# Optimization experiments

Measured on AMD Instinct MI355X. Metric: run time of the kernel, lower is better.

## Reference

```python
import jax, jax.numpy as jnp
from jax import lax
import numpy as np

NZ = 1000        # latent / probability-vector size
TRUNC = 50       # self.truncation
C = 50.0         # self.c
EPS = 1e-5       # BatchNorm eps (PyTorch default)


def _conv_transpose(x, w, b, stride, pad):
    """PyTorch ConvTranspose2d. w: (in_ch, out_ch, kh, kw), x: NCHW."""
    k = w.shape[2]
    # flip spatially, swap in/out -> OIHW kernel for a dilated forward conv
    w_eff = jnp.transpose(jnp.flip(w, (2, 3)), (1, 0, 2, 3))
    p = k - 1 - pad
    y = lax.conv_general_dilated(
        x, w_eff, window_strides=(1, 1), padding=[(p, p), (p, p)],
        lhs_dilation=(stride, stride),
        dimension_numbers=("NCHW", "OIHW", "NCHW"))
    return y + b[None, :, None, None]


def _batchnorm(x, gamma, beta):
    # training-mode BN: batch statistics over (N, H, W), biased variance
    m = x.mean((0, 2, 3), keepdims=True)
    v = ((x - m) ** 2).mean((0, 2, 3), keepdims=True)
    xn = (x - m) * lax.rsqrt(v + EPS)
    return xn * gamma[None, :, None, None] + beta[None, :, None, None]


def setup_inputs() -> dict:
    key = jax.random.key(0)
    ks = jax.random.split(key, 8)
    B = 2048
    s = 0.02
    inp = {
        "x": jax.random.uniform(ks[0], (B, NZ), jnp.float32),
        "w1": jax.random.normal(ks[1], (NZ, 512, 4, 4), jnp.float32) * s,
        "b1": jnp.zeros((512,), jnp.float32),
        "g1": jnp.ones((512,), jnp.float32),
        "be1": jnp.zeros((512,), jnp.float32),
        "w2": jax.random.normal(ks[2], (512, 256, 4, 4), jnp.float32) * s,
        "b2": jnp.zeros((256,), jnp.float32),
        "g2": jnp.ones((256,), jnp.float32),
        "be2": jnp.zeros((256,), jnp.float32),
        "w3": jax.random.normal(ks[3], (256, 128, 4, 4), jnp.float32) * s,
        "b3": jnp.zeros((128,), jnp.float32),
        "g3": jnp.ones((128,), jnp.float32),
        "be3": jnp.zeros((128,), jnp.float32),
        "w4": jax.random.normal(ks[4], (128, 1, 4, 4), jnp.float32) * s,
        "b4": jnp.zeros((1,), jnp.float32),
    }
    return inp


def reference(x, w1, b1, g1, be1, w2, b2, g2, be2, w3, b3, g3, be3, w4, b4):
    B = x.shape[0]
    # truncation_vector: topk -> clamp(log)+c -> shift nonneg -> scatter
    top_k, idx = lax.top_k(x, TRUNC)                      # [B, TRUNC]
    top_k = jnp.maximum(jnp.log(top_k), -1000.0) + C
    top_k = top_k + jax.nn.relu(-top_k.min(1, keepdims=True))
    z = jnp.zeros((B, NZ), x.dtype).at[jnp.arange(B)[:, None], idx].set(top_k)

    h = z.reshape(B, NZ, 1, 1)
    h = jnp.tanh(_batchnorm(_conv_transpose(h, w1, b1, 1, 0), g1, be1))  # [B,512,4,4]
    h = jnp.tanh(_batchnorm(_conv_transpose(h, w2, b2, 2, 1), g2, be2))  # [B,256,8,8]
    h = jnp.tanh(_batchnorm(_conv_transpose(h, w3, b3, 2, 1), g3, be3))  # [B,128,16,16]
    h = jax.nn.sigmoid(_conv_transpose(h, w4, b4, 2, 1))                 # [B,1,32,32]
    return h.reshape(B, 1, 32, 32)
```

## Files before the change

### kernel.cpp

```cpp
#include <hip/hip_runtime.h>
#include <cstdint>
#include <cstddef>


typedef unsigned short u16;
typedef unsigned int u32;
typedef __attribute__((ext_vector_type(8))) short s16x8;
typedef __attribute__((ext_vector_type(16))) float f32x16;

static __device__ __forceinline__ float bf2f(u16 u) {
  union { u32 i; float f; } v; v.i = ((u32)u) << 16; return v.f;
}
static __device__ __forceinline__ u16 f2bf(float f) {
  union { float f; u32 i; } v; v.f = f;
  const u32 r = v.i + 0x7fffu + ((v.i >> 16) & 1u);
  return (u16)(r >> 16);
}
static __device__ __forceinline__ void lds_barrier() {
  asm volatile("s_waitcnt lgkmcnt(0)" ::: "memory");
  __builtin_amdgcn_s_barrier();
}

__global__ __launch_bounds__(256) void topk_kernel(const float* __restrict__ x,
                                                   float* __restrict__ vals,
                                                   int* __restrict__ idxs) {
  const int lane = threadIdx.x & 63;
  const int b = blockIdx.x * 4 + (threadIdx.x >> 6);
  float v[16];
  #pragma unroll
  for (int j = 0; j < 16; ++j) {
    const int idx = lane + 64 * j;
    v[j] = (idx < 1000) ? x[(size_t)b * 1000 + idx] : -INFINITY;
  }
  float keepv = 1.0f;
  int keepi = 0;
  for (int k = 0; k < 50; ++k) {
    float bv = v[0]; int bj = 0;
    #pragma unroll
    for (int j = 1; j < 16; ++j)
      if (v[j] > bv) { bv = v[j]; bj = j; }
    int bi = lane + 64 * bj;
    #pragma unroll
    for (int off = 1; off < 64; off <<= 1) {
      const float ov = __shfl_xor(bv, off);
      const int oi = __shfl_xor(bi, off);
      if (ov > bv || (ov == bv && oi < bi)) { bv = ov; bi = oi; }
    }
    const int slot = bi >> 6;
    const bool own = (lane == (bi & 63));
    #pragma unroll
    for (int j = 0; j < 16; ++j)
      if (own && slot == j) v[j] = -INFINITY;
    if (lane == k) { keepv = bv; keepi = bi; }
  }
  const float tk = fmaxf(logf(keepv), -1000.0f) + 50.0f;
  float m = (lane < 50) ? tk : INFINITY;
  #pragma unroll
  for (int off = 1; off < 64; off <<= 1) m = fminf(m, __shfl_xor(m, off));
  const float shift = fmaxf(-m, 0.0f);
  if (lane < 50) {
    vals[b * 50 + lane] = tk + shift;
    idxs[b * 50 + lane] = keepi;
  }
}

__global__ __launch_bounds__(256) void w1t_kernel(const float* __restrict__ w1,
                                                  u16* __restrict__ w1t) {
  const int cin = blockIdx.x;
  const int t = threadIdx.x;
  __shared__ float is[512 * 17];
  const float* src = w1 + (size_t)cin * 8192;
  #pragma unroll
  for (int r = 0; r < 8; ++r) {
    const int f = r * 1024 + t * 4;
    const float4 v = *reinterpret_cast<const float4*>(src + f);
    const int co = f >> 4, s = f & 15;
    is[co * 17 + s + 0] = v.x;
    is[co * 17 + s + 1] = v.y;
    is[co * 17 + s + 2] = v.z;
    is[co * 17 + s + 3] = v.w;
  }
  __syncthreads();
  u16* dst = w1t + (size_t)cin * 8192;
  #pragma unroll
  for (int p = 0; p < 4; ++p) {
    const int i8 = (p * 256 + t) * 8;
    const int s = i8 >> 9, co = i8 & 511;
    union { u16 h[8]; s16x8 v; } pk;
    #pragma unroll
    for (int q = 0; q < 8; ++q) pk.h[q] = f2bf(is[(co + q) * 17 + s]);
    *reinterpret_cast<s16x8*>(dst + i8) = pk.v;
  }
}

template <int CIN, int COUT>
__global__ __launch_bounds__(256) void wt2_kernel(const float* __restrict__ w,
                                                  u16* __restrict__ wt2,
                                                  int obase, int NCH) {
  constexpr int KB = CIN / 16;
  const int kb = blockIdx.x;
  const int chg = blockIdx.y;
  const int t = threadIdx.x;
  __shared__ __align__(16) u16 tile[16 * 32 * 16];
  for (int i = t; i < 512; i += 256) {
    const int kk = i >> 5;
    const int ch = i & 31;
    const float* src = w + ((size_t)(kb * 16 + kk) * COUT + obase + chg * 32 + ch) * 16;
    #pragma unroll
    for (int q4 = 0; q4 < 4; ++q4) {
      const float4 v = *reinterpret_cast<const float4*>(src + q4 * 4);
      tile[(q4 * 4 + 0) * 512 + ch * 16 + kk] = f2bf(v.x);
      tile[(q4 * 4 + 1) * 512 + ch * 16 + kk] = f2bf(v.y);
      tile[(q4 * 4 + 2) * 512 + ch * 16 + kk] = f2bf(v.z);
      tile[(q4 * 4 + 3) * 512 + ch * 16 + kk] = f2bf(v.w);
    }
  }
  __syncthreads();
  for (int i = t; i < 16 * 64; i += 256) {
    const int tap = i >> 6;
    const int off = (i & 63) * 8;
    u16* dst = wt2 + ((size_t)(tap * KB + kb) * NCH + chg * 32) * 16 + off;
    *reinterpret_cast<s16x8*>(dst) = *reinterpret_cast<const s16x8*>(tile + tap * 512 + off);
  }
}

__global__ __launch_bounds__(256) void conv1_kernel(const float* __restrict__ vals,
                                                    const int* __restrict__ idxs,
                                                    const u16* __restrict__ w1t,
                                                    const float* __restrict__ b1,
                                                    u16* __restrict__ y1) {
  const int b = blockIdx.x;
  const int t = threadIdx.x;
  __shared__ float sval[50];
  __shared__ int sidx[50];
  if (t < 50) { sval[t] = vals[b * 50 + t]; sidx[t] = idxs[b * 50 + t]; }
  __syncthreads();
  const int co = (t & 63) * 8;
  const int s0 = t >> 6;
  float b8[8];
  #pragma unroll
  for (int q = 0; q < 8; ++q) b8[q] = b1[co + q];
  #pragma unroll
  for (int sp = 0; sp < 4; ++sp) {
    const int s = sp * 4 + s0;
    float acc[8] = {0.f, 0.f, 0.f, 0.f, 0.f, 0.f, 0.f, 0.f};
    for (int j = 0; j < 50; ++j) {
      const float v = sval[j];
      union { s16x8 v8; u16 h[8]; } w;
      w.v8 = *reinterpret_cast<const s16x8*>(w1t + (size_t)sidx[j] * 8192 + s * 512 + co);
      #pragma unroll
      for (int q = 0; q < 8; ++q) acc[q] = fmaf(v, bf2f(w.h[q]), acc[q]);
    }
    union { u16 h[8]; s16x8 v8; } o;
    #pragma unroll
    for (int q = 0; q < 8; ++q) o.h[q] = f2bf(acc[q] + b8[q]);
    *reinterpret_cast<s16x8*>(y1 + (size_t)b * 8192 + s * 512 + co) = o.v8;
  }
}

__global__ __launch_bounds__(256) void bnstats_kernel(const u16* __restrict__ y,
                                                      float* __restrict__ sp,
                                                      float* __restrict__ sqp,
                                                      int C, int CB, int ROWS) {
  const int PB = CB >> 1;
  const int PR = 256 / PB;
  const int t = threadIdx.x;
  const int cp = t & (PB - 1);
  const int rl = t / PB;
  const int cbase = blockIdx.x * CB;
  const int split = blockIdx.y;
  const int RPB = ROWS >> 7;
  const u16* base = y + (size_t)split * RPB * C + cbase + 2 * cp;
  float s0 = 0.f, s1 = 0.f, q0 = 0.f, q1 = 0.f;
  for (int r = rl; r < RPB; r += PR) {
    const u32 raw = *reinterpret_cast<const u32*>(base + (size_t)r * C);
    const float a = bf2f((u16)(raw & 0xffffu));
    const float b = bf2f((u16)(raw >> 16));
    s0 += a; s1 += b;
    q0 = fmaf(a, a, q0); q1 = fmaf(b, b, q1);
  }
  __shared__ float4 arr[256];
  arr[t] = make_float4(s0, s1, q0, q1);
  __syncthreads();
  if (t < PB) {
    float4 acc = arr[t];
    for (int g = 1; g < PR; ++g) {
      const float4 v = arr[g * PB + t];
      acc.x += v.x; acc.y += v.y; acc.z += v.z; acc.w += v.w;
    }
    const int c = cbase + 2 * t;
    sp[split * C + c] = acc.x;
    sp[split * C + c + 1] = acc.y;
    sqp[split * C + c] = acc.z;
    sqp[split * C + c + 1] = acc.w;
  }
}

__global__ __launch_bounds__(256) void bnfin_kernel(const float* __restrict__ sp,
                                                    const float* __restrict__ sqp,
                                                    const float* __restrict__ g,
                                                    const float* __restrict__ be,
                                                    float* __restrict__ a,
                                                    float* __restrict__ bb,
                                                    int logC, int SPLITS, float inv) {
  const int t = threadIdx.x;
  const int C = 1 << logC;
  const int lc = t & (C - 1);
  int PARTS = 256 >> logC;
  if (PARTS == 0) PARTS = 1;
  const int part = (logC >= 8) ? 0 : (t >> logC);
  const int chunk = SPLITS / PARTS;
  const int c = (blockIdx.x << 8) + lc;
  float s = 0.f, s2 = 0.f;
  for (int k = part * chunk; k < (part + 1) * chunk; ++k) {
    s += sp[(size_t)k * C + c];
    s2 += sqp[(size_t)k * C + c];
  }
  __shared__ float rs[256], rq[256];
  rs[t] = s; rq[t] = s2;
  __syncthreads();
  if (part == 0 && t < C) {
    for (int p = 1; p < PARTS; ++p) {
      s += rs[(p << logC) + lc];
      s2 += rq[(p << logC) + lc];
    }
    const float m = s * inv;
    float var = fmaf(-m, m, s2 * inv);
    var = fmaxf(var, 0.f);
    const float r = 1.0f / sqrtf(var + 1e-5f);
    const float av = g[c] * r;
    a[c] = av;
    bb[c] = fmaf(-m, av, be[c]);
  }
}

__global__ __launch_bounds__(256) void bnact_kernel(u16* __restrict__ y,
                                                    const float* __restrict__ a,
                                                    const float* __restrict__ bb,
                                                    int Cm1) {
  const size_t i = ((size_t)blockIdx.x * 256 + threadIdx.x) * 8;
  const int c = (int)i & Cm1;
  uint4 raw = *reinterpret_cast<uint4*>(y + i);
  float av[8], bv[8];
  *reinterpret_cast<float4*>(av) = *reinterpret_cast<const float4*>(a + c);
  *reinterpret_cast<float4*>(av + 4) = *reinterpret_cast<const float4*>(a + c + 4);
  *reinterpret_cast<float4*>(bv) = *reinterpret_cast<const float4*>(bb + c);
  *reinterpret_cast<float4*>(bv + 4) = *reinterpret_cast<const float4*>(bb + c + 4);
  u32 w[4] = {raw.x, raw.y, raw.z, raw.w};
  #pragma unroll
  for (int q = 0; q < 4; ++q) {
    const float lo = tanhf(fmaf(bf2f((u16)(w[q] & 0xffffu)), av[2 * q], bv[2 * q]));
    const float hi = tanhf(fmaf(bf2f((u16)(w[q] >> 16)), av[2 * q + 1], bv[2 * q + 1]));
    w[q] = (u32)f2bf(lo) | ((u32)f2bf(hi) << 16);
  }
  raw.x = w[0]; raw.y = w[1]; raw.z = w[2]; raw.w = w[3];
  *reinterpret_cast<uint4*>(y + i) = raw;
}

template <int SIN, int CIN, int WM, int WN, int MBATCH, int COUT_STORE>
__global__ __launch_bounds__(512, 2) void convt_mfma(const u16* __restrict__ in,
                                                     const u16* __restrict__ wt,
                                                     const float* __restrict__ bias,
                                                     u16* __restrict__ outp,
                                                     float* __restrict__ spp,
                                                     float* __restrict__ sqpp,
                                                     int o_gbase) {
  constexpr int SS = SIN * SIN;
  constexpr int MB = MBATCH * SS;
  constexpr int NB = WN * 32;
  constexpr int KB = CIN / 16;
  constexpr int LOGS = (SIN == 4) ? 2 : 3;
  constexpr int NPASS = MB / 64;
  constexpr int NSTEP = CIN / 64;
  constexpr int BUFW = (MB + 1) * 64;
  constexpr int KYT[2][2] = {{1, 3}, {2, 0}};
  constexpr int DYT[2][2] = {{0, -1}, {0, 1}};
  static_assert(WM * WN == 8, "8 waves");
  static_assert(MB == WM * 32, "MFR==1");
  __shared__ __align__(16) u16 As[2 * BUFW];
  __shared__ float sred[512];

  const int t = threadIdx.x;
  const int lane = t & 63;
  const int wave = t >> 6;
  const int wn = wave % WN;
  const int wm = wave / WN;
  const int l31 = lane & 31;
  const int kl2 = lane >> 5;
  const int bx = blockIdx.x;
  const int R0 = blockIdx.y * MB;
  const int NCHT = gridDim.x * NB;

  int rb[9];
  {
    const int r = wm * 32 + l31;
    const int bl = r >> (2 * LOGS);
    const int rr = r & (SS - 1);
    const int sy = rr >> LOGS, sx = rr & (SIN - 1);
    #pragma unroll
    for (int dyi = 0; dyi < 3; ++dyi)
      #pragma unroll
      for (int dxi = 0; dxi < 3; ++dxi) {
        const int ny = sy + dyi - 1, nx = sx + dxi - 1;
        const bool ok = (ny >= 0 && ny < SIN && nx >= 0 && nx < SIN);
        const int rp = ok ? ((bl << (2 * LOGS)) + (ny << LOGS) + nx) : MB;
        rb[dyi * 3 + dxi] = (rp << 7) | ((rp & 7) << 4);
      }
  }
  if (t < 16) {
    s16x8 z = {};
    const int buf = t >> 3;
    *reinterpret_cast<s16x8*>(As + buf * BUFW + MB * 64 + (t & 7) * 8) = z;
  }

  f32x16 acc[2][2];
  #pragma unroll
  for (int py = 0; py < 2; ++py)
    #pragma unroll
    for (int px = 0; px < 2; ++px) acc[py][px] = (f32x16)(0.f);

  const int chb = bx * NB + wn * 32;
  const int ocw = chb + l31;
  const u16* wlane = wt + (size_t)(chb + l31) * 16 + kl2 * 8;
  const size_t nstride = (size_t)NCHT * 16;

  const int srow = t >> 3;
  const int scol = (t & 7) * 8;
  const u16* gsrc = in + (size_t)(R0 + srow) * CIN + scol;

  s16x8 sreg[NPASS];
  #pragma unroll
  for (int p = 0; p < NPASS; ++p)
    sreg[p] = *reinterpret_cast<const s16x8*>(gsrc + (size_t)p * 64 * CIN);

  int cur = 0;
  for (int s = 0; s < NSTEP; ++s) {
    u16* dbuf = As + cur * BUFW;
    #pragma unroll
    for (int p = 0; p < NPASS; ++p) {
      const int row = p * 64 + srow;
      const int db = row * 128 + ((scol * 2) ^ ((row & 7) << 4));
      *reinterpret_cast<s16x8*>((char*)dbuf + db) = sreg[p];
    }
    if (s + 1 < NSTEP) {
      const u16* gn = gsrc + (s + 1) * 64;
      #pragma unroll
      for (int p = 0; p < NPASS; ++p)
        sreg[p] = *reinterpret_cast<const s16x8*>(gn + (size_t)p * 64 * CIN);
    }
    lds_barrier();

    const u16* Ab = As + cur * BUFW;
    #pragma unroll
    for (int ksub = 0; ksub < 4; ++ksub) {
      const int kb = s * 4 + ksub;
      s16x8 bf[2][2][2][2];
      #pragma unroll
      for (int py = 0; py < 2; ++py)
        #pragma unroll
        for (int px = 0; px < 2; ++px)
          #pragma unroll
          for (int jy = 0; jy < 2; ++jy)
            #pragma unroll
            for (int jx = 0; jx < 2; ++jx) {
              const int tap = KYT[py][jy] * 4 + KYT[px][jx];
              bf[py][px][jy][jx] = *reinterpret_cast<const s16x8*>(
                  wlane + (size_t)(tap * KB + kb) * nstride);
            }
      const int koff = ksub * 32 + kl2 * 16;
      s16x8 af[9];
      #pragma unroll
      for (int s9 = 0; s9 < 9; ++s9)
        af[s9] = *reinterpret_cast<const s16x8*>((const char*)Ab + (rb[s9] ^ koff));
      __builtin_amdgcn_s_setprio(1);
      #pragma unroll
      for (int py = 0; py < 2; ++py)
        #pragma unroll
        for (int px = 0; px < 2; ++px)
          #pragma unroll
          for (int jy = 0; jy < 2; ++jy)
            #pragma unroll
            for (int jx = 0; jx < 2; ++jx) {
              const int s9 = (DYT[py][jy] + 1) * 3 + (DYT[px][jx] + 1);
              acc[py][px] = __builtin_amdgcn_mfma_f32_32x32x16_bf16(
                  af[s9], bf[py][px][jy][jx], acc[py][px], 0, 0, 0);
            }
      __builtin_amdgcn_s_setprio(0);
    }
    cur ^= 1;
  }

  const float bo = bias[o_gbase + ocw];
  const int B0 = blockIdx.y * MBATCH;
  float s_ = 0.f, q_ = 0.f;
  #pragma unroll
  for (int i = 0; i < 16; ++i) {
    const int rl_ = (i & 3) + 8 * (i >> 2) + 4 * kl2;
    const int r = wm * 32 + rl_;
    const int bl = r >> (2 * LOGS);
    const int rr = r & (SS - 1);
    const int sy = rr >> LOGS, sx = rr & (SIN - 1);
    const size_t ob = (size_t)(B0 + bl) * 4 * SS;
    #pragma unroll
    for (int py = 0; py < 2; ++py)
      #pragma unroll
      for (int px = 0; px < 2; ++px) {
        const int od = (2 * sy + py) * (2 * SIN) + 2 * sx + px;
        const float v = acc[py][px][i] + bo;
        s_ += v;
        q_ = fmaf(v, v, q_);
        outp[(ob + od) * COUT_STORE + ocw] = f2bf(v);
      }
  }
  s_ += __shfl_xor(s_, 32);
  q_ += __shfl_xor(q_, 32);
  if (lane < 32) {
    sred[wave * 32 + l31] = s_;
    sred[256 + wave * 32 + l31] = q_;
  }
  __syncthreads();
  if (t < WN * 32) {
    const int wnr = t >> 5;
    const int ch = t & 31;
    float ss = 0.f, qq = 0.f;
    #pragma unroll
    for (int w = 0; w < WM; ++w) {
      ss += sred[(w * WN + wnr) * 32 + ch];
      qq += sred[256 + (w * WN + wnr) * 32 + ch];
    }
    const int c = bx * NB + wnr * 32 + ch;
    spp[(size_t)blockIdx.y * COUT_STORE + c] = ss;
    sqpp[(size_t)blockIdx.y * COUT_STORE + c] = qq;
  }
}

__global__ __launch_bounds__(256) void conv4_kernel(const u16* __restrict__ h3c,
                                                    const float* __restrict__ ac,
                                                    const float* __restrict__ bc,
                                                    const float* __restrict__ w4,
                                                    const float* __restrict__ b4,
                                                    float* __restrict__ outp,
                                                    int cbase, int last) {
  const int b = blockIdx.x;
  const int t = threadIdx.x;
  __shared__ float wsh[32 * 16];
  __shared__ float is[32 * 257];
  for (int i = t; i < 512; i += 256) wsh[i] = w4[cbase * 16 + i];
  const int cq = (t & 3) * 8;
  float av[8], bv[8];
  *reinterpret_cast<float4*>(av)     = *reinterpret_cast<const float4*>(ac + cq);
  *reinterpret_cast<float4*>(av + 4) = *reinterpret_cast<const float4*>(ac + cq + 4);
  *reinterpret_cast<float4*>(bv)     = *reinterpret_cast<const float4*>(bc + cq);
  *reinterpret_cast<float4*>(bv + 4) = *reinterpret_cast<const float4*>(bc + cq + 4);
  #pragma unroll
  for (int p = 0; p < 4; ++p) {
    const int idx8 = p * 256 + t;
    const int s = idx8 >> 2;
    union { s16x8 v8; u16 h[8]; } r;
    r.v8 = *reinterpret_cast<const s16x8*>(h3c + ((size_t)b * 256 + s) * 32 + cq);
    #pragma unroll
    for (int q = 0; q < 8; ++q)
      is[(cq + q) * 257 + s] = tanhf(fmaf(bf2f(r.h[q]), av[q], bv[q]));
  }
  __syncthreads();
  float acc[4] = {0.f, 0.f, 0.f, 0.f};
  const int ox = t & 31;
  const int oy0 = t >> 5;
  for (int c = 0; c < 32; ++c) {
    #pragma unroll
    for (int k = 0; k < 4; ++k) {
      const int oy = oy0 + 8 * k;
      #pragma unroll
      for (int jy = 0; jy < 2; ++jy) {
        const int ky = 2 * jy + 1 - (oy & 1);
        const int iyn = oy + 1 - ky;
        if ((unsigned)iyn < 32u) {
          const int iy = iyn >> 1;
          #pragma unroll
          for (int jx = 0; jx < 2; ++jx) {
            const int kx = 2 * jx + 1 - (ox & 1);
            const int ixn = ox + 1 - kx;
            if ((unsigned)ixn < 32u) {
              const int ix = ixn >> 1;
              acc[k] = fmaf(is[c * 257 + iy * 16 + ix], wsh[c * 16 + ky * 4 + kx], acc[k]);
            }
          }
        }
      }
    }
  }
  #pragma unroll
  for (int k = 0; k < 4; ++k) {
    const int oy = oy0 + 8 * k;
    const size_t ob = (size_t)b * 1024 + oy * 32 + ox;
    const float base = (cbase == 0) ? b4[0] : outp[ob];
    const float v = base + acc[k];
    outp[ob] = last ? (1.0f / (1.0f + expf(-v))) : v;
  }
}

extern "C" void kernel_launch(void* const* d_in, const int* in_sizes, int n_in,
                              void* d_out, int out_size, void* d_ws, size_t ws_size,
                              hipStream_t stream) {
  (void)in_sizes; (void)n_in; (void)out_size; (void)ws_size;
  const float* x   = (const float*)d_in[0];
  const float* w1  = (const float*)d_in[1];
  const float* b1  = (const float*)d_in[2];
  const float* g1  = (const float*)d_in[3];
  const float* be1 = (const float*)d_in[4];
  const float* w2  = (const float*)d_in[5];
  const float* b2  = (const float*)d_in[6];
  const float* g2  = (const float*)d_in[7];
  const float* be2 = (const float*)d_in[8];
  const float* w3  = (const float*)d_in[9];
  const float* b3  = (const float*)d_in[10];
  const float* g3  = (const float*)d_in[11];
  const float* be3 = (const float*)d_in[12];
  const float* w4  = (const float*)d_in[13];
  const float* b4  = (const float*)d_in[14];

  char* ws = (char*)d_ws;
  u16*   y2   = (u16*)(ws + 0);
  u16*   y1   = (u16*)(ws + 67108864);
  u16*   y3c  = (u16*)(ws + 100663296);
  u16*   w1t  = (u16*)(ws + 100663296);
  u16*   w2t  = (u16*)(ws + 117047296);
  float* vals = (float*)(ws + 134217728);
  int*   idxs = (int*)(ws + 134627328);
  float* sp   = (float*)(ws + 134217728);
  float* sqp  = (float*)(ws + 134479872);
  float* ac   = (float*)(ws + 134742016);
  float* bc   = (float*)(ws + 134744064);
  u16*   w3tc = (u16*)(ws + 134746112);
  float* outp = (float*)d_out;

  w1t_kernel<<<1000, 256, 0, stream>>>(w1, w1t);
  wt2_kernel<512, 256><<<dim3(32, 8), 256, 0, stream>>>(w2, w2t, 0, 256);
  topk_kernel<<<512, 256, 0, stream>>>(x, vals, idxs);

  conv1_kernel<<<2048, 256, 0, stream>>>(vals, idxs, w1t, b1, y1);
  bnstats_kernel<<<dim3(4, 128), 256, 0, stream>>>(y1, sp, sqp, 512, 128, 32768);
  bnfin_kernel<<<2, 256, 0, stream>>>(sp, sqp, g1, be1, ac, bc, 9, 128, 1.0f / 32768.0f);
  bnact_kernel<<<8192, 256, 0, stream>>>(y1, ac, bc, 511);

  convt_mfma<4, 512, 4, 2, 8, 256><<<dim3(4, 256), 512, 0, stream>>>(
      y1, w2t, b2, y2, sp, sqp, 0);
  bnfin_kernel<<<1, 256, 0, stream>>>(sp, sqp, g2, be2, ac, bc, 8, 256, 1.0f / 131072.0f);
  bnact_kernel<<<16384, 256, 0, stream>>>(y2, ac, bc, 255);

  for (int ch = 0; ch < 4; ++ch) {
    const int cb = ch * 32;
    wt2_kernel<256, 128><<<dim3(16, 1), 256, 0, stream>>>(w3, w3tc, cb, 32);
    convt_mfma<8, 256, 8, 1, 4, 32><<<dim3(1, 512), 512, 0, stream>>>(
        y2, w3tc, b3, y3c, sp, sqp, cb);
    bnfin_kernel<<<1, 256, 0, stream>>>(sp, sqp, g3 + cb, be3 + cb, ac, bc, 5, 512,
                                        1.0f / 524288.0f);
    conv4_kernel<<<2048, 256, 0, stream>>>(y3c, ac, bc, w4, b4, outp, cb, ch == 3);
  }
}
```

Baseline: 1.120 ms.

## Shrink MFMA conv tiles to 4 waves, software-pipeline B loads, chunk layer3 by 64

The transposed-conv MFMA kernel now uses 256-thread blocks (4 waves) with smaller M tiles, giving more blocks. Weight fragments are loaded per output phase with double-buffered prefetch instead of all 16 up front, which lowers register pressure. Layer 3 is processed in two 64-channel chunks instead of four 32-channel chunks, with BN statistics moved to a separate bnstats pass and conv4 templated on channel count. Smaller tiles give less reuse of weights per block, and the extra stats kernel adds another read of y3c.

After: 1.510 ms. +34.8%, slower.

```diff
diff --git a/kernel.cpp b/kernel.cpp
--- a/kernel.cpp
+++ b/kernel.cpp
@@ -161,7 +161,7 @@
 __global__ __launch_bounds__(256) void bnstats_kernel(const u16* __restrict__ y,
                                                       float* __restrict__ sp,
                                                       float* __restrict__ sqp,
-                                                      int C, int CB, int ROWS) {
+                                                      int C, int CB, long long ROWS) {
   const int PB = CB >> 1;
   const int PR = 256 / PB;
   const int t = threadIdx.x;
@@ -169,10 +169,10 @@
   const int rl = t / PB;
   const int cbase = blockIdx.x * CB;
   const int split = blockIdx.y;
-  const int RPB = ROWS >> 7;
+  const long long RPB = ROWS >> 7;
   const u16* base = y + (size_t)split * RPB * C + cbase + 2 * cp;
   float s0 = 0.f, s1 = 0.f, q0 = 0.f, q1 = 0.f;
-  for (int r = rl; r < RPB; r += PR) {
+  for (long long r = rl; r < RPB; r += PR) {
     const u32 raw = *reinterpret_cast<const u32*>(base + (size_t)r * C);
     const float a = bf2f((u16)(raw & 0xffffu));
     const float b = bf2f((u16)(raw >> 16));
@@ -257,28 +257,28 @@
   *reinterpret_cast<uint4*>(y + i) = raw;
 }
 
-template <int SIN, int CIN, int WM, int WN, int MBATCH, int COUT_STORE>
-__global__ __launch_bounds__(512, 2) void convt_mfma(const u16* __restrict__ in,
-                                                     const u16* __restrict__ wt,
-                                                     const float* __restrict__ bias,
-                                                     u16* __restrict__ outp,
-                                                     float* __restrict__ spp,
-                                                     float* __restrict__ sqpp,
-                                                     int o_gbase) {
+template <int SIN, int CIN, int WM, int WN, int MBATCH, int COUT_STORE, bool STATS>
+__global__ __launch_bounds__(256) void convt_mfma(const u16* __restrict__ in,
+                                                  const u16* __restrict__ wt,
+                                                  const float* __restrict__ bias,
+                                                  u16* __restrict__ outp,
+                                                  float* __restrict__ spp,
+                                                  float* __restrict__ sqpp,
+                                                  int o_gbase) {
   constexpr int SS = SIN * SIN;
   constexpr int MB = MBATCH * SS;
   constexpr int NB = WN * 32;
   constexpr int KB = CIN / 16;
   constexpr int LOGS = (SIN == 4) ? 2 : 3;
-  constexpr int NPASS = MB / 64;
+  constexpr int NPASS = MB / 32;
   constexpr int NSTEP = CIN / 64;
   constexpr int BUFW = (MB + 1) * 64;
   constexpr int KYT[2][2] = {{1, 3}, {2, 0}};
   constexpr int DYT[2][2] = {{0, -1}, {0, 1}};
-  static_assert(WM * WN == 8, "8 waves");
+  static_assert(WM * WN == 4, "4 waves");
   static_assert(MB == WM * 32, "MFR==1");
   __shared__ __align__(16) u16 As[2 * BUFW];
-  __shared__ float sred[512];
+  __shared__ float sred[256];
 
   const int t = threadIdx.x;
   const int lane = t & 63;
@@ -331,14 +331,14 @@
   s16x8 sreg[NPASS];
   #pragma unroll
   for (int p = 0; p < NPASS; ++p)
-    sreg[p] = *reinterpret_cast<const s16x8*>(gsrc + (size_t)p * 64 * CIN);
+    sreg[p] = *reinterpret_cast<const s16x8*>(gsrc + (size_t)p * 32 * CIN);
 
   int cur = 0;
   for (int s = 0; s < NSTEP; ++s) {
     u16* dbuf = As + cur * BUFW;
     #pragma unroll
     for (int p = 0; p < NPASS; ++p) {
-      const int row = p * 64 + srow;
+      const int row = p * 32 + srow;
       const int db = row * 128 + ((scol * 2) ^ ((row & 7) << 4));
       *reinterpret_cast<s16x8*>((char*)dbuf + db) = sreg[p];
     }
@@ -346,7 +346,7 @@
       const u16* gn = gsrc + (s + 1) * 64;
       #pragma unroll
       for (int p = 0; p < NPASS; ++p)
-        sreg[p] = *reinterpret_cast<const s16x8*>(gn + (size_t)p * 64 * CIN);
+        sreg[p] = *reinterpret_cast<const s16x8*>(gn + (size_t)p * 32 * CIN);
     }
     lds_barrier();
 
@@ -354,38 +354,43 @@
     #pragma unroll
     for (int ksub = 0; ksub < 4; ++ksub) {
       const int kb = s * 4 + ksub;
-      s16x8 bf[2][2][2][2];
-      #pragma unroll
-      for (int py = 0; py < 2; ++py)
-        #pragma unroll
-        for (int px = 0; px < 2; ++px)
-          #pragma unroll
-          for (int jy = 0; jy < 2; ++jy)
-            #pragma unroll
-            for (int jx = 0; jx < 2; ++jx) {
-              const int tap = KYT[py][jy] * 4 + KYT[px][jx];
-              bf[py][px][jy][jx] = *reinterpret_cast<const s16x8*>(
-                  wlane + (size_t)(tap * KB + kb) * nstride);
-            }
+      const u16* wkb = wlane + (size_t)kb * nstride;
       const int koff = ksub * 32 + kl2 * 16;
       s16x8 af[9];
       #pragma unroll
       for (int s9 = 0; s9 < 9; ++s9)
         af[s9] = *reinterpret_cast<const s16x8*>((const char*)Ab + (rb[s9] ^ koff));
-      __builtin_amdgcn_s_setprio(1);
-      #pragma unroll
-      for (int py = 0; py < 2; ++py)
+      s16x8 bq0[4], bq1[4];
+      #pragma unroll
+      for (int j = 0; j < 4; ++j) {
+        const int tap = KYT[0][j >> 1] * 4 + KYT[0][j & 1];
+        bq0[j] = *reinterpret_cast<const s16x8*>(wkb + (size_t)tap * KB * nstride);
+      }
+      #pragma unroll
+      for (int q = 0; q < 4; ++q) {
+        const int py = q >> 1, px = q & 1;
+        if (q < 3) {
+          const int nq = q + 1;
+          const int npy = nq >> 1, npx = nq & 1;
+          s16x8* nb = (nq & 1) ? bq1 : bq0;
+          #pragma unroll
+          for (int j = 0; j < 4; ++j) {
+            const int tap = KYT[npy][j >> 1] * 4 + KYT[npx][j & 1];
+            nb[j] = *reinterpret_cast<const s16x8*>(wkb + (size_t)tap * KB * nstride);
+          }
+        }
+        const s16x8* cb = (q & 1) ? bq1 : bq0;
+        __builtin_amdgcn_s_setprio(1);
         #pragma unroll
-        for (int px = 0; px < 2; ++px)
+        for (int jy = 0; jy < 2; ++jy)
           #pragma unroll
-          for (int jy = 0; jy < 2; ++jy)
-            #pragma unroll
-            for (int jx = 0; jx < 2; ++jx) {
-              const int s9 = (DYT[py][jy] + 1) * 3 + (DYT[px][jx] + 1);
-              acc[py][px] = __builtin_amdgcn_mfma_f32_32x32x16_bf16(
-                  af[s9], bf[py][px][jy][jx], acc[py][px], 0, 0, 0);
-            }
-      __builtin_amdgcn_s_setprio(0);
+          for (int jx = 0; jx < 2; ++jx) {
+            const int s9 = (DYT[py][jy] + 1) * 3 + (DYT[px][jx] + 1);
+            acc[py][px] = __builtin_amdgcn_mfma_f32_32x32x16_bf16(
+                af[s9], cb[jy * 2 + jx], acc[py][px], 0, 0, 0);
+          }
+        __builtin_amdgcn_s_setprio(0);
+      }
     }
     cur ^= 1;
   }
@@ -412,28 +417,31 @@
         outp[(ob + od) * COUT_STORE + ocw] = f2bf(v);
       }
   }
-  s_ += __shfl_xor(s_, 32);
-  q_ += __shfl_xor(q_, 32);
-  if (lane < 32) {
-    sred[wave * 32 + l31] = s_;
-    sred[256 + wave * 32 + l31] = q_;
-  }
-  __syncthreads();
-  if (t < WN * 32) {
-    const int wnr = t >> 5;
-    const int ch = t & 31;
-    float ss = 0.f, qq = 0.f;
-    #pragma unroll
-    for (int w = 0; w < WM; ++w) {
-      ss += sred[(w * WN + wnr) * 32 + ch];
-      qq += sred[256 + (w * WN + wnr) * 32 + ch];
-    }
-    const int c = bx * NB + wnr * 32 + ch;
-    spp[(size_t)blockIdx.y * COUT_STORE + c] = ss;
-    sqpp[(size_t)blockIdx.y * COUT_STORE + c] = qq;
-  }
-}
-
+  if constexpr (STATS) {
+    s_ += __shfl_xor(s_, 32);
+    q_ += __shfl_xor(q_, 32);
+    if (lane < 32) {
+      sred[wave * 32 + l31] = s_;
+      sred[128 + wave * 32 + l31] = q_;
+    }
+    __syncthreads();
+    if (t < WN * 32) {
+      const int wnr = t >> 5;
+      const int ch = t & 31;
+      float ss = 0.f, qq = 0.f;
+      #pragma unroll
+      for (int w = 0; w < WM; ++w) {
+        ss += sred[(w * WN + wnr) * 32 + ch];
+        qq += sred[128 + (w * WN + wnr) * 32 + ch];
+      }
+      const int c = bx * NB + wnr * 32 + ch;
+      spp[(size_t)blockIdx.y * COUT_STORE + c] = ss;
+      sqpp[(size_t)blockIdx.y * COUT_STORE + c] = qq;
+    }
+  }
+}
+
+template <int NCH>
 __global__ __launch_bounds__(256) void conv4_kernel(const u16* __restrict__ h3c,
                                                     const float* __restrict__ ac,
                                                     const float* __restrict__ bc,
@@ -443,21 +451,22 @@
                                                     int cbase, int last) {
   const int b = blockIdx.x;
   const int t = threadIdx.x;
-  __shared__ float wsh[32 * 16];
-  __shared__ float is[32 * 257];
-  for (int i = t; i < 512; i += 256) wsh[i] = w4[cbase * 16 + i];
-  const int cq = (t & 3) * 8;
+  __shared__ float wsh[NCH * 16];
+  __shared__ float is[NCH * 257];
+  for (int i = t; i < NCH * 16; i += 256) wsh[i] = w4[cbase * 16 + i];
+  constexpr int CG = NCH / 8;
+  const int cq = (t & (CG - 1)) * 8;
   float av[8], bv[8];
   *reinterpret_cast<float4*>(av)     = *reinterpret_cast<const float4*>(ac + cq);
   *reinterpret_cast<float4*>(av + 4) = *reinterpret_cast<const float4*>(ac + cq + 4);
   *reinterpret_cast<float4*>(bv)     = *reinterpret_cast<const float4*>(bc + cq);
   *reinterpret_cast<float4*>(bv + 4) = *reinterpret_cast<const float4*>(bc + cq + 4);
   #pragma unroll
-  for (int p = 0; p < 4; ++p) {
-    const int idx8 = p * 256 + t;
-    const int s = idx8 >> 2;
+  for (int p = 0; p < CG; ++p) {
+    const int i8 = p * 256 + t;
+    const int s = i8 / CG;
     union { s16x8 v8; u16 h[8]; } r;
-    r.v8 = *reinterpret_cast<const s16x8*>(h3c + ((size_t)b * 256 + s) * 32 + cq);
+    r.v8 = *reinterpret_cast<const s16x8*>(h3c + ((size_t)b * 256 + s) * NCH + cq);
     #pragma unroll
     for (int q = 0; q < 8; ++q)
       is[(cq + q) * 257 + s] = tanhf(fmaf(bf2f(r.h[q]), av[q], bv[q]));
@@ -466,7 +475,7 @@
   float acc[4] = {0.f, 0.f, 0.f, 0.f};
   const int ox = t & 31;
   const int oy0 = t >> 5;
-  for (int c = 0; c < 32; ++c) {
+  for (int c = 0; c < NCH; ++c) {
     #pragma unroll
     for (int k = 0; k < 4; ++k) {
       const int oy = oy0 + 8 * k;
@@ -522,16 +531,20 @@
   char* ws = (char*)d_ws;
   u16*   y2   = (u16*)(ws + 0);
   u16*   y1   = (u16*)(ws + 67108864);
-  u16*   y3c  = (u16*)(ws + 100663296);
+  u16*   y3c  = (u16*)(ws + 67108864);
   u16*   w1t  = (u16*)(ws + 100663296);
+  float* sp2  = (float*)(ws + 100663296);
+  float* sqp2 = (float*)(ws + 101187584);
   u16*   w2t  = (u16*)(ws + 117047296);
   float* vals = (float*)(ws + 134217728);
   int*   idxs = (int*)(ws + 134627328);
-  float* sp   = (float*)(ws + 134217728);
-  float* sqp  = (float*)(ws + 134479872);
+  float* sp1  = (float*)(ws + 134217728);
+  float* sqp1 = (float*)(ws + 134479872);
+  u16*   w3tc = (u16*)(ws + 134217728);
   float* ac   = (float*)(ws + 134742016);
   float* bc   = (float*)(ws + 134744064);
-  u16*   w3tc = (u16*)(ws + 134746112);
+  float* sp3  = (float*)(ws + 134746112);
+  float* sqp3 = (float*)(ws + 134778880);
   float* outp = (float*)d_out;
 
   w1t_kernel<<<1000, 256, 0, stream>>>(w1, w1t);
@@ -539,22 +552,23 @@
   topk_kernel<<<512, 256, 0, stream>>>(x, vals, idxs);
 
   conv1_kernel<<<2048, 256, 0, stream>>>(vals, idxs, w1t, b1, y1);
-  bnstats_kernel<<<dim3(4, 128), 256, 0, stream>>>(y1, sp, sqp, 512, 128, 32768);
-  bnfin_kernel<<<2, 256, 0, stream>>>(sp, sqp, g1, be1, ac, bc, 9, 128, 1.0f / 32768.0f);
+  bnstats_kernel<<<dim3(4, 128), 256, 0, stream>>>(y1, sp1, sqp1, 512, 128, 32768);
+  bnfin_kernel<<<2, 256, 0, stream>>>(sp1, sqp1, g1, be1, ac, bc, 9, 128, 1.0f / 32768.0f);
   bnact_kernel<<<8192, 256, 0, stream>>>(y1, ac, bc, 511);
 
-  convt_mfma<4, 512, 4, 2, 8, 256><<<dim3(4, 256), 512, 0, stream>>>(
-      y1, w2t, b2, y2, sp, sqp, 0);
-  bnfin_kernel<<<1, 256, 0, stream>>>(sp, sqp, g2, be2, ac, bc, 8, 256, 1.0f / 131072.0f);
+  convt_mfma<4, 512, 2, 2, 4, 256, true><<<dim3(4, 512), 256, 0, stream>>>(
+      y1, w2t, b2, y2, sp2, sqp2, 0);
+  bnfin_kernel<<<1, 256, 0, stream>>>(sp2, sqp2, g2, be2, ac, bc, 8, 512, 1.0f / 131072.0f);
   bnact_kernel<<<16384, 256, 0, stream>>>(y2, ac, bc, 255);
 
-  for (int ch = 0; ch < 4; ++ch) {
-    const int cb = ch * 32;
-    wt2_kernel<256, 128><<<dim3(16, 1), 256, 0, stream>>>(w3, w3tc, cb, 32);
-    convt_mfma<8, 256, 8, 1, 4, 32><<<dim3(1, 512), 512, 0, stream>>>(
-        y2, w3tc, b3, y3c, sp, sqp, cb);
-    bnfin_kernel<<<1, 256, 0, stream>>>(sp, sqp, g3 + cb, be3 + cb, ac, bc, 5, 512,
+  for (int ch = 0; ch < 2; ++ch) {
+    const int cb = ch * 64;
+    wt2_kernel<256, 128><<<dim3(16, 2), 256, 0, stream>>>(w3, w3tc, cb, 64);
+    convt_mfma<8, 256, 2, 2, 1, 64, false><<<dim3(1, 2048), 256, 0, stream>>>(
+        y2, w3tc, b3, y3c, sp3, sqp3, cb);
+    bnstats_kernel<<<dim3(1, 128), 256, 0, stream>>>(y3c, sp3, sqp3, 64, 64, 524288LL);
+    bnfin_kernel<<<1, 256, 0, stream>>>(sp3, sqp3, g3 + cb, be3 + cb, ac, bc, 6, 128,
                                         1.0f / 524288.0f);
-    conv4_kernel<<<2048, 256, 0, stream>>>(y3c, ac, bc, w4, b4, outp, cb, ch == 3);
-  }
-}
+    conv4_kernel<64><<<2048, 256, 0, stream>>>(y3c, ac, bc, w4, b4, outp, cb, ch == 1);
+  }
+}
```
